# Optimization experiments

Measured on AMD Instinct MI355X. Metric: run time of the kernel, lower is better.

## Reference

```python
import jax, jax.numpy as jnp
import numpy as np

N_USERS = 100_000
N_ITEMS = 50_000
N_EDGES = 2_000_000
D = 64
ALPHA = 0.5      # tanh-blend coefficient (alpha)
NORM_2 = -1.0    # exponent on back-aggregation degree norm (args.norm_2)


def setup_inputs() -> dict:
    key = jax.random.key(0)
    k1, k2, k3, k4, k5 = jax.random.split(key, 5)
    return {
        "h_user": jax.random.normal(k1, (N_USERS, D), jnp.float32) * 0.1,
        "pretrained_feature": jax.random.normal(k2, (N_ITEMS, D), jnp.float32),
        "edge_w": jax.random.normal(k3, (N_ITEMS, 1), jnp.float32),
        "src_idx": jax.random.randint(k4, (N_EDGES,), 0, N_USERS, dtype=jnp.int32),
        "dst_idx": jax.random.randint(k5, (N_EDGES,), 0, N_ITEMS, dtype=jnp.int32),
    }


def reference(h_user, pretrained_feature, edge_w, src_idx, dst_idx):
    # HGCNLayer.forward: bidirectional copy_src+sum aggregation with degree norm,
    # tanh prompt blend and node-softmax edge weighting.
    ones = jnp.ones((N_EDGES,), h_user.dtype)

    # forward pass user -> item: rst[d] = sum_{(s,d) in E} h_user[s]
    rst = jax.ops.segment_sum(h_user[src_idx], dst_idx, num_segments=N_ITEMS)  # [N_ITEMS, D]
    deg_dst = jnp.clip(jax.ops.segment_sum(ones, dst_idx, num_segments=N_ITEMS), 1.0)

    # alpha * tanh prompt blend
    rst = rst + ALPHA * jnp.tanh(pretrained_feature)
    # edge-prompt softmax scaling (softmax over nodes; see notes)
    rst = jax.nn.softmax(edge_w, axis=0) * rst
    # in-degree^-1 normalization
    rst = rst / deg_dst[:, None]

    # backward pass item -> user: bsrc[s] = sum_{(s,d) in E} rst[d]
    bsrc = jax.ops.segment_sum(rst[dst_idx], src_idx, num_segments=N_USERS)  # [N_USERS, D]
    deg_src = jnp.clip(jax.ops.segment_sum(ones, src_idx, num_segments=N_USERS), 1.0)
    bsrc = bsrc * jnp.power(deg_src, NORM_2)[:, None]
    return bsrc
```

## Files before the change

### kernel.cpp

```cpp
#include <hip/hip_runtime.h>
#include <hip/hip_bf16.h>
#include <math.h>

#define N_USERS 100000
#define N_ITEMS 50000
#define N_EDGES 2000000
#define D 64

#define FB_BINS 98
#define BB_BINS 196
#define NBINS   (FB_BINS + BB_BINS)
#define CHUNK   4096
#define NCHUNK  ((N_EDGES + CHUNK - 1) / CHUNK)
#define FOFF_F_N (FB_BINS * 1024 + 1)
#define FOFF_B_N (BB_BINS * 512 + 1)
#define TOTSLOT  (2 * N_EDGES)
#define FWD_WGS (N_ITEMS / 16)
#define BWD_WGS ((N_USERS + 15) / 16)
#define SHARD_SPLIT 50000

__device__ __forceinline__ float blo(unsigned u) {
    union { unsigned i; float f; } c; c.i = u << 16; return c.f;
}
__device__ __forceinline__ float bhi(unsigned u) {
    union { unsigned i; float f; } c; c.i = u & 0xFFFF0000u; return c.f;
}
__device__ __forceinline__ unsigned bpack(float x, float y) {
    __hip_bfloat16 a = __float2bfloat16(x), b = __float2bfloat16(y);
    unsigned short ua = *reinterpret_cast<unsigned short*>(&a);
    unsigned short ub = *reinterpret_cast<unsigned short*>(&b);
    return (unsigned)ua | ((unsigned)ub << 16);
}

__device__ __forceinline__ void gather_run(
    const unsigned* __restrict__ tbl, const unsigned* __restrict__ stage2,
    int a, int b, int q, int half, float& ax, float& ay) {
    int k = a;
    for (; k + 16 <= b; k += 16) {
        int s0 = (int)__builtin_nontemporal_load(&stage2[k + half]);
        int s1 = (int)__builtin_nontemporal_load(&stage2[k + 2 + half]);
        int s2 = (int)__builtin_nontemporal_load(&stage2[k + 4 + half]);
        int s3 = (int)__builtin_nontemporal_load(&stage2[k + 6 + half]);
        int s4 = (int)__builtin_nontemporal_load(&stage2[k + 8 + half]);
        int s5 = (int)__builtin_nontemporal_load(&stage2[k + 10 + half]);
        int s6 = (int)__builtin_nontemporal_load(&stage2[k + 12 + half]);
        int s7 = (int)__builtin_nontemporal_load(&stage2[k + 14 + half]);
        unsigned u0 = tbl[(s0 << 5) + q];
        unsigned u1 = tbl[(s1 << 5) + q];
        unsigned u2 = tbl[(s2 << 5) + q];
        unsigned u3 = tbl[(s3 << 5) + q];
        unsigned u4 = tbl[(s4 << 5) + q];
        unsigned u5 = tbl[(s5 << 5) + q];
        unsigned u6 = tbl[(s6 << 5) + q];
        unsigned u7 = tbl[(s7 << 5) + q];
        ax += ((blo(u0) + blo(u1)) + (blo(u2) + blo(u3)))
            + ((blo(u4) + blo(u5)) + (blo(u6) + blo(u7)));
        ay += ((bhi(u0) + bhi(u1)) + (bhi(u2) + bhi(u3)))
            + ((bhi(u4) + bhi(u5)) + (bhi(u6) + bhi(u7)));
    }
    if (k + 8 <= b) {
        int s0 = (int)__builtin_nontemporal_load(&stage2[k + half]);
        int s1 = (int)__builtin_nontemporal_load(&stage2[k + 2 + half]);
        int s2 = (int)__builtin_nontemporal_load(&stage2[k + 4 + half]);
        int s3 = (int)__builtin_nontemporal_load(&stage2[k + 6 + half]);
        unsigned u0 = tbl[(s0 << 5) + q];
        unsigned u1 = tbl[(s1 << 5) + q];
        unsigned u2 = tbl[(s2 << 5) + q];
        unsigned u3 = tbl[(s3 << 5) + q];
        ax += (blo(u0) + blo(u1)) + (blo(u2) + blo(u3));
        ay += (bhi(u0) + bhi(u1)) + (bhi(u2) + bhi(u3));
        k += 8;
    }
    for (; k + 2 <= b; k += 2) {
        unsigned u = tbl[((int)__builtin_nontemporal_load(&stage2[k + half]) << 5) + q];
        ax += blo(u); ay += bhi(u);
    }
    if (k < b && half == 0) {
        unsigned u = tbl[((int)__builtin_nontemporal_load(&stage2[k]) << 5) + q];
        ax += blo(u); ay += bhi(u);
    }
}

__global__ __launch_bounds__(256) void prep_kernel(
    const float2* __restrict__ hin, unsigned* __restrict__ hu16,
    const int* __restrict__ src, const int* __restrict__ dst,
    int* __restrict__ gh) {
    __shared__ int h[NBINS];
    for (int i = threadIdx.x; i < NBINS; i += 256) h[i] = 0;
    __syncthreads();
    int stride = gridDim.x * blockDim.x;
    int t0 = blockIdx.x * blockDim.x + threadIdx.x;
    for (int i = t0; i < N_USERS * 32; i += stride) {
        float2 v = hin[i];
        hu16[i] = bpack(v.x, v.y);
    }
    for (int e = t0; e < N_EDGES; e += stride) {
        atomicAdd(&h[dst[e] >> 9], 1);
        atomicAdd(&h[FB_BINS + (src[e] >> 9)], 1);
    }
    __syncthreads();
    for (int i = threadIdx.x; i < NBINS; i += 256) {
        int v = h[i];
        if (v) atomicAdd(&gh[i], v);
    }
}

__global__ void scan_soft_kernel(const int* __restrict__ in, int* __restrict__ out,
                                 int* __restrict__ cur,
                                 const float* __restrict__ w, float* __restrict__ stats) {
    __shared__ float redf[16];
    __shared__ int wsum[16];
    int tid = threadIdx.x, lane = tid & 63, wid = tid >> 6;

    if (blockIdx.x == 0) {
        int idx0 = tid * 4;
        int v[4]; int tot = 0;
#pragma unroll
        for (int e = 0; e < 4; e++) {
            int i = idx0 + e;
            v[e] = (i < NBINS) ? in[i] : 0;
            tot += v[e];
        }
        int incl = tot;
#pragma unroll
        for (int off = 1; off < 64; off <<= 1) {
            int t = __shfl_up(incl, off);
            if (lane >= off) incl += t;
        }
        if (lane == 63) wsum[wid] = incl;
        __syncthreads();
        if (wid == 0 && lane < 16) {
            int t = wsum[lane];
            int sc = t;
#pragma unroll
            for (int off = 1; off < 16; off <<= 1) {
                int u = __shfl_up(sc, off);
                if (lane >= off) sc += u;
            }
            wsum[lane] = sc - t;
        }
        __syncthreads();
        int excl = wsum[wid] + incl - tot;
#pragma unroll
        for (int e = 0; e < 4; e++) {
            int i = idx0 + e;
            if (i < NBINS) { out[i] = excl; cur[i] = excl; }
            if (i == NBINS) out[i] = excl;
            excl += v[e];
        }
        return;
    }

    float m = -INFINITY;
    for (int i = tid; i < N_ITEMS; i += 1024) m = fmaxf(m, w[i]);
#pragma unroll
    for (int off = 32; off; off >>= 1) m = fmaxf(m, __shfl_xor(m, off));
    if (lane == 0) redf[wid] = m;
    __syncthreads();
    if (tid == 0) {
        float t = redf[0];
        for (int k = 1; k < 16; k++) t = fmaxf(t, redf[k]);
        redf[0] = t;
    }
    __syncthreads();
    m = redf[0];
    __syncthreads();

    float s = 0.f;
    for (int i = tid; i < N_ITEMS; i += 1024) s += expf(w[i] - m);
#pragma unroll
    for (int off = 32; off; off >>= 1) s += __shfl_xor(s, off);
    if (lane == 0) redf[wid] = s;
    __syncthreads();
    if (tid == 0) {
        float t = 0.f;
        for (int k = 0; k < 16; k++) t += redf[k];
        stats[0] = m;
        stats[1] = t;
    }
}

__global__ __launch_bounds__(256) void binfill_kernel(
    const int* __restrict__ src, const int* __restrict__ dst,
    int* __restrict__ gcur, unsigned* __restrict__ stage) {
    __shared__ int cnt[NBINS];
    __shared__ int gbase[NBINS];
    __shared__ int lcur[NBINS];
    int c = blockIdx.x;
    int base = c * CHUNK;
    int nEdge = N_EDGES - base; if (nEdge > CHUNK) nEdge = CHUNK;

    for (int t = threadIdx.x; t < NBINS; t += 256) { cnt[t] = 0; lcur[t] = 0; }
    __syncthreads();

    int es[16], ed[16];
#pragma unroll
    for (int j = 0; j < 16; j++) {
        int k = j * 256 + threadIdx.x;
        if (k < nEdge) {
            es[j] = src[base + k];
            ed[j] = dst[base + k];
            atomicAdd(&cnt[ed[j] >> 9], 1);
            atomicAdd(&cnt[FB_BINS + (es[j] >> 9)], 1);
        } else {
            es[j] = -1;
        }
    }
    __syncthreads();
    for (int t = threadIdx.x; t < NBINS; t += 256) {
        int cv = cnt[t];
        gbase[t] = cv ? atomicAdd(&gcur[t], cv) : 0;
    }
    __syncthreads();
#pragma unroll
    for (int j = 0; j < 16; j++) {
        if (es[j] >= 0) {
            int s = es[j], d = ed[j];
            int bf = d >> 9;
            int p = atomicAdd(&lcur[bf], 1);
            stage[gbase[bf] + p] = (unsigned)s | ((unsigned)(d & 511) << 17);
            int bb = FB_BINS + (s >> 9);
            int q = atomicAdd(&lcur[bb], 1);
            stage[gbase[bb] + q] = (unsigned)d | ((unsigned)(s & 511) << 16);
        }
    }
}

__global__ __launch_bounds__(512) void redist3_kernel(
    const unsigned* __restrict__ stage, const int* __restrict__ binoff,
    unsigned* __restrict__ stage2, int* __restrict__ foff_f, int* __restrict__ foff_b) {
    __shared__ int cnt[1024];
    __shared__ int wsum[8];
    int wg = blockIdx.x, t = threadIdx.x, lane = t & 63, wv = t >> 6;

    if (wg < FB_BINS) {
        int B = wg;
        int beg = binoff[B], end = binoff[B + 1];
        cnt[t] = 0; cnt[t + 512] = 0;
        __syncthreads();
        for (int k = beg + t; k < end; k += 512) {
            unsigned e = stage[k];
            int key = (int)((e >> 17) & 511) << 1;
            key |= ((e & 0x1FFFFu) >= SHARD_SPLIT) ? 1 : 0;
            atomicAdd(&cnt[key], 1);
        }
        __syncthreads();
        int c0 = cnt[t << 1], c1 = cnt[(t << 1) | 1];
        int v = c0 + c1;
        int incl = v;
#pragma unroll
        for (int off = 1; off < 64; off <<= 1) {
            int u = __shfl_up(incl, off);
            if (lane >= off) incl += u;
        }
        if (lane == 63) wsum[wv] = incl;
        __syncthreads();
        if (t == 0) {
            int run = 0;
#pragma unroll
            for (int k2 = 0; k2 < 8; k2++) { int x = wsum[k2]; wsum[k2] = run; run += x; }
        }
        __syncthreads();
        int base = beg + wsum[wv] + incl - v;
        int slot = (B << 10) | (t << 1);
        foff_f[slot] = base;
        foff_f[slot | 1] = base + c0;
        cnt[t << 1] = base;
        cnt[(t << 1) | 1] = base + c0;
        if (B == FB_BINS - 1 && t == 0) foff_f[FB_BINS * 1024] = end;
        __syncthreads();
        for (int k = beg + t; k < end; k += 512) {
            unsigned e = stage[k];
            int key = (int)((e >> 17) & 511) << 1;
            key |= ((e & 0x1FFFFu) >= SHARD_SPLIT) ? 1 : 0;
            int p = atomicAdd(&cnt[key], 1);
            stage2[p] = e & 0x1FFFFu;
        }
    } else {
        for (int pass = 0; pass < 2; pass++) {
            int B = FB_BINS + ((wg - FB_BINS) << 1) + pass;
            int beg = binoff[B], end = binoff[B + 1];
            cnt[t] = 0;
            __syncthreads();
            for (int k = beg + t; k < end; k += 512) {
                unsigned e = stage[k];
                atomicAdd(&cnt[(e >> 16) & 511], 1);
            }
            __syncthreads();
            int v = cnt[t];
            int incl = v;
#pragma unroll
            for (int off = 1; off < 64; off <<= 1) {
                int u = __shfl_up(incl, off);
                if (lane >= off) incl += u;
            }
            if (lane == 63) wsum[wv] = incl;
            __syncthreads();
            if (t == 0) {
                int run = 0;
#pragma unroll
                for (int k2 = 0; k2 < 8; k2++) { int x = wsum[k2]; wsum[k2] = run; run += x; }
            }
            __syncthreads();
            int base = beg + wsum[wv] + incl - v;
            foff_b[((B - FB_BINS) << 9) | t] = base;
            cnt[t] = base;
            if (B == NBINS - 1 && t == 0) foff_b[BB_BINS * 512] = end;
            __syncthreads();
            for (int k = beg + t; k < end; k += 512) {
                unsigned e = stage[k];
                int p = atomicAdd(&cnt[(e >> 16) & 511], 1);
                stage2[p] = e & 0xFFFFu;
            }
            __syncthreads();
        }
    }
}

__global__ __launch_bounds__(256) void fwd_s0_kernel(
    const unsigned* __restrict__ hu16, const unsigned* __restrict__ stage2,
    const int* __restrict__ foff_f, float* __restrict__ pacc) {
    int tid = threadIdx.x, lane = tid & 63, wv = tid >> 6;
    int q = lane & 31, half = lane >> 5;
    int i0 = blockIdx.x * 16;

    for (int il = wv; il < 16; il += 4) {
        int i = i0 + il;
        if (i >= N_ITEMS) break;
        int a = foff_f[i << 1], b = foff_f[(i << 1) | 1];
        float ax = 0.f, ay = 0.f;
        gather_run(hu16, stage2, a, b, q, half, ax, ay);
        ax += __shfl_xor(ax, 32);
        ay += __shfl_xor(ay, 32);
        if (half == 0) {
            size_t off = ((size_t)i * 32 + q) * 2;
            __builtin_nontemporal_store(ax, &pacc[off]);
            __builtin_nontemporal_store(ay, &pacc[off + 1]);
        }
    }
}

__global__ __launch_bounds__(256) void fwd_s1_kernel(
    const unsigned* __restrict__ hu16, const float* __restrict__ pf,
    const float* __restrict__ edge_w, const unsigned* __restrict__ stage2,
    const int* __restrict__ foff_f, const float* __restrict__ stats,
    const float* __restrict__ pacc, unsigned* __restrict__ rst16) {
    int tid = threadIdx.x, lane = tid & 63, wv = tid >> 6;
    int q = lane & 31, half = lane >> 5;
    float m = stats[0], ssum = stats[1];
    const float2* PF2 = (const float2*)pf;
    int i0 = blockIdx.x * 16;

    for (int il = wv; il < 16; il += 4) {
        int i = i0 + il;
        if (i >= N_ITEMS) break;
        int a = foff_f[(i << 1) | 1], b = foff_f[(i << 1) + 2];
        int a0 = foff_f[i << 1];
        float ax = 0.f, ay = 0.f;
        gather_run(hu16, stage2, a, b, q, half, ax, ay);
        ax += __shfl_xor(ax, 32);
        ay += __shfl_xor(ay, 32);
        if (half == 0) {
            size_t off = ((size_t)i * 32 + q) * 2;
            float px = __builtin_nontemporal_load(&pacc[off]);
            float py = __builtin_nontemporal_load(&pacc[off + 1]);
            ax += px; ay += py;
            float deg = (float)(b - a0);
            if (deg < 1.f) deg = 1.f;
            float sc = expf(edge_w[i] - m) / (ssum * deg);
            float2 pv = PF2[(size_t)i * 32 + q];
            float vx = (ax + 0.5f * tanhf(pv.x)) * sc;
            float vy = (ay + 0.5f * tanhf(pv.y)) * sc;
            rst16[(size_t)i * 32 + q] = bpack(vx, vy);
        }
    }
}

__global__ __launch_bounds__(256) void bwd_gather_kernel(
    const unsigned* __restrict__ rst16, const unsigned* __restrict__ stage2,
    const int* __restrict__ foff_b, float* __restrict__ out) {
    int tid = threadIdx.x, lane = tid & 63, wv = tid >> 6;
    int q = lane & 31, half = lane >> 5;
    float2* OUT2 = (float2*)out;
    int u0i = blockIdx.x * 16;

    for (int il = wv; il < 16; il += 4) {
        int u = u0i + il;
        if (u >= N_USERS) break;
        int a = foff_b[u], b = foff_b[u + 1];
        float ax = 0.f, ay = 0.f;
        gather_run(rst16, stage2, a, b, q, half, ax, ay);
        ax += __shfl_xor(ax, 32);
        ay += __shfl_xor(ay, 32);
        if (half == 0) {
            float deg = (float)(b - a);
            if (deg < 1.f) deg = 1.f;
            OUT2[(size_t)u * 32 + q] = make_float2(ax / deg, ay / deg);
        }
    }
}

extern "C" void kernel_launch(void* const* d_in, const int* in_sizes, int n_in,
                              void* d_out, int out_size, void* d_ws, size_t ws_size,
                              hipStream_t stream) {
    const float* h_user = (const float*)d_in[0];
    const float* pf     = (const float*)d_in[1];
    const float* edge_w = (const float*)d_in[2];
    const int*   src    = (const int*)d_in[3];
    const int*   dst    = (const int*)d_in[4];
    float* out = (float*)d_out;

    char* p = (char*)d_ws;
    int* gh      = (int*)p;     p += sizeof(int) * NBINS;
    int* binoff  = (int*)p;     p += sizeof(int) * (NBINS + 1);
    int* gcur    = (int*)p;     p += sizeof(int) * NBINS;
    int* foff_f  = (int*)p;     p += sizeof(int) * FOFF_F_N;
    int* foff_b  = (int*)p;     p += sizeof(int) * FOFF_B_N;
    float* stats = (float*)p;   p += 4 * sizeof(float);
    unsigned* stage  = (unsigned*)p; p += sizeof(unsigned) * (size_t)TOTSLOT;
    unsigned* stage2 = (unsigned*)p; p += sizeof(unsigned) * (size_t)TOTSLOT;
    unsigned* hu16   = (unsigned*)p; p += sizeof(unsigned) * (size_t)N_USERS * 32;
    unsigned* rst16  = (unsigned*)p; p += sizeof(unsigned) * (size_t)N_ITEMS * 32;
    float* pacc      = (float*)p;    p += sizeof(float) * (size_t)N_ITEMS * 64;

    hipMemsetAsync(gh, 0, sizeof(int) * NBINS, stream);

    prep_kernel<<<1024, 256, 0, stream>>>((const float2*)h_user, hu16, src, dst, gh);
    scan_soft_kernel<<<2, 1024, 0, stream>>>(gh, binoff, gcur, edge_w, stats);
    binfill_kernel<<<NCHUNK, 256, 0, stream>>>(src, dst, gcur, stage);
    redist3_kernel<<<196, 512, 0, stream>>>(stage, binoff, stage2, foff_f, foff_b);
    fwd_s0_kernel<<<FWD_WGS, 256, 0, stream>>>(hu16, stage2, foff_f, pacc);
    fwd_s1_kernel<<<FWD_WGS, 256, 0, stream>>>(hu16, pf, edge_w, stage2, foff_f, stats, pacc, rst16);
    bwd_gather_kernel<<<BWD_WGS, 256, 0, stream>>>(rst16, stage2, foff_b, out);
}
```

Before: 346.4 us.

## Fuse preprocessing chain into one cooperative kernel and merge forward gather shards

Four preprocessing kernels (histogram/bf16 pack, scan+softmax stats, bin fill, redistribution) become a single cooperative kernel that separates its phases with grid.sync, so the per-launch gaps between them go away. The forward gather no longer splits each item's edges into two source shards with a partial-accumulator buffer. It is now one gather kernel per item, which drops the pacc round trip and one launch. The trade-offs are grid-wide barriers, a fixed 512-block grid that loops over chunks, and the loss of the shard split that may have aided cache locality on the h_user table.

```diff
diff --git a/kernel.cpp b/kernel.cpp
--- a/kernel.cpp
+++ b/kernel.cpp
@@ -1,6 +1,9 @@
 #include <hip/hip_runtime.h>
+#include <hip/hip_cooperative_groups.h>
 #include <hip/hip_bf16.h>
 #include <math.h>
+
+namespace cg = cooperative_groups;
 
 #define N_USERS 100000
 #define N_ITEMS 50000
@@ -12,12 +15,13 @@
 #define NBINS   (FB_BINS + BB_BINS)
 #define CHUNK   4096
 #define NCHUNK  ((N_EDGES + CHUNK - 1) / CHUNK)
-#define FOFF_F_N (FB_BINS * 1024 + 1)
+#define FOFF_F_N (FB_BINS * 512 + 1)
 #define FOFF_B_N (BB_BINS * 512 + 1)
 #define TOTSLOT  (2 * N_EDGES)
+#define CHAIN_WGS 512
+#define CHAIN_THR 512
 #define FWD_WGS (N_ITEMS / 16)
 #define BWD_WGS ((N_USERS + 15) / 16)
-#define SHARD_SPLIT 50000
 
 __device__ __forceinline__ float blo(unsigned u) {
     union { unsigned i; float f; } c; c.i = u << 16; return c.f;
@@ -81,235 +85,203 @@
     }
 }
 
-__global__ __launch_bounds__(256) void prep_kernel(
+__global__ __launch_bounds__(CHAIN_THR, 4) void chain_kernel(
     const float2* __restrict__ hin, unsigned* __restrict__ hu16,
     const int* __restrict__ src, const int* __restrict__ dst,
-    int* __restrict__ gh) {
-    __shared__ int h[NBINS];
-    for (int i = threadIdx.x; i < NBINS; i += 256) h[i] = 0;
+    int* __restrict__ gh, int* __restrict__ binoff, int* __restrict__ gcur,
+    const float* __restrict__ w, float* __restrict__ stats,
+    unsigned* __restrict__ stage, unsigned* __restrict__ stage2,
+    int* __restrict__ foff_f, int* __restrict__ foff_b) {
+    cg::grid_group grid = cg::this_grid();
+    __shared__ int shA[1024];
+    __shared__ int shW[8];
+    __shared__ float shF[8];
+    int tid = threadIdx.x, lane = tid & 63, wv = tid >> 6;
+    int bx = blockIdx.x;
+    int gs = gridDim.x * CHAIN_THR;
+    int g0 = bx * CHAIN_THR + tid;
+
+    for (int i = tid; i < NBINS; i += CHAIN_THR) shA[i] = 0;
     __syncthreads();
-    int stride = gridDim.x * blockDim.x;
-    int t0 = blockIdx.x * blockDim.x + threadIdx.x;
-    for (int i = t0; i < N_USERS * 32; i += stride) {
+    for (int i = g0; i < N_USERS * 32; i += gs) {
         float2 v = hin[i];
         hu16[i] = bpack(v.x, v.y);
     }
-    for (int e = t0; e < N_EDGES; e += stride) {
-        atomicAdd(&h[dst[e] >> 9], 1);
-        atomicAdd(&h[FB_BINS + (src[e] >> 9)], 1);
+    for (int e = g0; e < N_EDGES; e += gs) {
+        atomicAdd(&shA[dst[e] >> 9], 1);
+        atomicAdd(&shA[FB_BINS + (src[e] >> 9)], 1);
     }
     __syncthreads();
-    for (int i = threadIdx.x; i < NBINS; i += 256) {
-        int v = h[i];
+    for (int i = tid; i < NBINS; i += CHAIN_THR) {
+        int v = shA[i];
         if (v) atomicAdd(&gh[i], v);
     }
-}
-
-__global__ void scan_soft_kernel(const int* __restrict__ in, int* __restrict__ out,
-                                 int* __restrict__ cur,
-                                 const float* __restrict__ w, float* __restrict__ stats) {
-    __shared__ float redf[16];
-    __shared__ int wsum[16];
-    int tid = threadIdx.x, lane = tid & 63, wid = tid >> 6;
-
-    if (blockIdx.x == 0) {
-        int idx0 = tid * 4;
-        int v[4]; int tot = 0;
-#pragma unroll
-        for (int e = 0; e < 4; e++) {
-            int i = idx0 + e;
-            v[e] = (i < NBINS) ? in[i] : 0;
-            tot += v[e];
-        }
-        int incl = tot;
+    grid.sync();
+
+    if (bx == 0) {
+        int v = (tid < NBINS) ? gh[tid] : 0;
+        int incl = v;
 #pragma unroll
         for (int off = 1; off < 64; off <<= 1) {
             int t = __shfl_up(incl, off);
             if (lane >= off) incl += t;
         }
-        if (lane == 63) wsum[wid] = incl;
-        __syncthreads();
-        if (wid == 0 && lane < 16) {
-            int t = wsum[lane];
+        if (lane == 63) shW[wv] = incl;
+        __syncthreads();
+        if (wv == 0 && lane < 8) {
+            int t = shW[lane];
             int sc = t;
 #pragma unroll
-            for (int off = 1; off < 16; off <<= 1) {
+            for (int off = 1; off < 8; off <<= 1) {
                 int u = __shfl_up(sc, off);
                 if (lane >= off) sc += u;
             }
-            wsum[lane] = sc - t;
-        }
-        __syncthreads();
-        int excl = wsum[wid] + incl - tot;
-#pragma unroll
-        for (int e = 0; e < 4; e++) {
-            int i = idx0 + e;
-            if (i < NBINS) { out[i] = excl; cur[i] = excl; }
-            if (i == NBINS) out[i] = excl;
-            excl += v[e];
-        }
-        return;
-    }
-
-    float m = -INFINITY;
-    for (int i = tid; i < N_ITEMS; i += 1024) m = fmaxf(m, w[i]);
-#pragma unroll
-    for (int off = 32; off; off >>= 1) m = fmaxf(m, __shfl_xor(m, off));
-    if (lane == 0) redf[wid] = m;
-    __syncthreads();
-    if (tid == 0) {
-        float t = redf[0];
-        for (int k = 1; k < 16; k++) t = fmaxf(t, redf[k]);
-        redf[0] = t;
-    }
-    __syncthreads();
-    m = redf[0];
-    __syncthreads();
-
-    float s = 0.f;
-    for (int i = tid; i < N_ITEMS; i += 1024) s += expf(w[i] - m);
-#pragma unroll
-    for (int off = 32; off; off >>= 1) s += __shfl_xor(s, off);
-    if (lane == 0) redf[wid] = s;
-    __syncthreads();
-    if (tid == 0) {
-        float t = 0.f;
-        for (int k = 0; k < 16; k++) t += redf[k];
-        stats[0] = m;
-        stats[1] = t;
-    }
-}
-
-__global__ __launch_bounds__(256) void binfill_kernel(
-    const int* __restrict__ src, const int* __restrict__ dst,
-    int* __restrict__ gcur, unsigned* __restrict__ stage) {
-    __shared__ int cnt[NBINS];
-    __shared__ int gbase[NBINS];
-    __shared__ int lcur[NBINS];
-    int c = blockIdx.x;
-    int base = c * CHUNK;
-    int nEdge = N_EDGES - base; if (nEdge > CHUNK) nEdge = CHUNK;
-
-    for (int t = threadIdx.x; t < NBINS; t += 256) { cnt[t] = 0; lcur[t] = 0; }
-    __syncthreads();
-
-    int es[16], ed[16];
-#pragma unroll
-    for (int j = 0; j < 16; j++) {
-        int k = j * 256 + threadIdx.x;
-        if (k < nEdge) {
-            es[j] = src[base + k];
-            ed[j] = dst[base + k];
-            atomicAdd(&cnt[ed[j] >> 9], 1);
-            atomicAdd(&cnt[FB_BINS + (es[j] >> 9)], 1);
-        } else {
-            es[j] = -1;
-        }
-    }
-    __syncthreads();
-    for (int t = threadIdx.x; t < NBINS; t += 256) {
-        int cv = cnt[t];
-        gbase[t] = cv ? atomicAdd(&gcur[t], cv) : 0;
-    }
-    __syncthreads();
-#pragma unroll
-    for (int j = 0; j < 16; j++) {
-        if (es[j] >= 0) {
-            int s = es[j], d = ed[j];
-            int bf = d >> 9;
-            int p = atomicAdd(&lcur[bf], 1);
-            stage[gbase[bf] + p] = (unsigned)s | ((unsigned)(d & 511) << 17);
-            int bb = FB_BINS + (s >> 9);
-            int q = atomicAdd(&lcur[bb], 1);
-            stage[gbase[bb] + q] = (unsigned)d | ((unsigned)(s & 511) << 16);
-        }
-    }
-}
-
-__global__ __launch_bounds__(512) void redist3_kernel(
-    const unsigned* __restrict__ stage, const int* __restrict__ binoff,
-    unsigned* __restrict__ stage2, int* __restrict__ foff_f, int* __restrict__ foff_b) {
-    __shared__ int cnt[1024];
-    __shared__ int wsum[8];
-    int wg = blockIdx.x, t = threadIdx.x, lane = t & 63, wv = t >> 6;
-
-    if (wg < FB_BINS) {
-        int B = wg;
+            shW[lane] = sc - t;
+        }
+        __syncthreads();
+        int excl = shW[wv] + incl - v;
+        if (tid < NBINS) { binoff[tid] = excl; gcur[tid] = excl; }
+        if (tid == NBINS - 1) binoff[NBINS] = excl + v;
+    } else if (bx == 1) {
+        float m = -INFINITY;
+        for (int i = tid; i < N_ITEMS; i += CHAIN_THR) m = fmaxf(m, w[i]);
+#pragma unroll
+        for (int off = 32; off; off >>= 1) m = fmaxf(m, __shfl_xor(m, off));
+        if (lane == 0) shF[wv] = m;
+        __syncthreads();
+        if (tid == 0) {
+            float t = shF[0];
+            for (int k = 1; k < 8; k++) t = fmaxf(t, shF[k]);
+            shF[0] = t;
+        }
+        __syncthreads();
+        m = shF[0];
+        __syncthreads();
+        float s = 0.f;
+        for (int i = tid; i < N_ITEMS; i += CHAIN_THR) s += expf(w[i] - m);
+#pragma unroll
+        for (int off = 32; off; off >>= 1) s += __shfl_xor(s, off);
+        if (lane == 0) shF[wv] = s;
+        __syncthreads();
+        if (tid == 0) {
+            float t = 0.f;
+            for (int k = 0; k < 8; k++) t += shF[k];
+            stats[0] = m;
+            stats[1] = t;
+        }
+    }
+    grid.sync();
+
+    {
+        int* cnt   = shA;
+        int* gbase = shA + 294;
+        int* lcur  = shA + 588;
+        for (int c = bx; c < NCHUNK; c += gridDim.x) {
+            int base = c * CHUNK;
+            int nEdge = N_EDGES - base; if (nEdge > CHUNK) nEdge = CHUNK;
+            for (int t = tid; t < NBINS; t += CHAIN_THR) { cnt[t] = 0; lcur[t] = 0; }
+            __syncthreads();
+            int es[8], ed[8];
+#pragma unroll
+            for (int j = 0; j < 8; j++) {
+                int k = j * CHAIN_THR + tid;
+                if (k < nEdge) {
+                    es[j] = src[base + k];
+                    ed[j] = dst[base + k];
+                    atomicAdd(&cnt[ed[j] >> 9], 1);
+                    atomicAdd(&cnt[FB_BINS + (es[j] >> 9)], 1);
+                } else {
+                    es[j] = -1;
+                }
+            }
+            __syncthreads();
+            for (int t = tid; t < NBINS; t += CHAIN_THR) {
+                int cv = cnt[t];
+                gbase[t] = cv ? atomicAdd(&gcur[t], cv) : 0;
+            }
+            __syncthreads();
+#pragma unroll
+            for (int j = 0; j < 8; j++) {
+                if (es[j] >= 0) {
+                    int s = es[j], d = ed[j];
+                    int bf = d >> 9;
+                    int p = atomicAdd(&lcur[bf], 1);
+                    stage[gbase[bf] + p] = (unsigned)s | ((unsigned)(d & 511) << 17);
+                    int bb = FB_BINS + (s >> 9);
+                    int qq = atomicAdd(&lcur[bb], 1);
+                    stage[gbase[bb] + qq] = (unsigned)d | ((unsigned)(s & 511) << 16);
+                }
+            }
+            __syncthreads();
+        }
+    }
+    grid.sync();
+
+    if (bx < FB_BINS) {
+        int B = bx;
         int beg = binoff[B], end = binoff[B + 1];
-        cnt[t] = 0; cnt[t + 512] = 0;
-        __syncthreads();
-        for (int k = beg + t; k < end; k += 512) {
-            unsigned e = stage[k];
-            int key = (int)((e >> 17) & 511) << 1;
-            key |= ((e & 0x1FFFFu) >= SHARD_SPLIT) ? 1 : 0;
-            atomicAdd(&cnt[key], 1);
-        }
-        __syncthreads();
-        int c0 = cnt[t << 1], c1 = cnt[(t << 1) | 1];
-        int v = c0 + c1;
+        shA[tid] = 0;
+        __syncthreads();
+        for (int k = beg + tid; k < end; k += CHAIN_THR)
+            atomicAdd(&shA[(stage[k] >> 17) & 511], 1);
+        __syncthreads();
+        int v = shA[tid];
         int incl = v;
 #pragma unroll
         for (int off = 1; off < 64; off <<= 1) {
             int u = __shfl_up(incl, off);
             if (lane >= off) incl += u;
         }
-        if (lane == 63) wsum[wv] = incl;
-        __syncthreads();
-        if (t == 0) {
+        if (lane == 63) shW[wv] = incl;
+        __syncthreads();
+        if (tid == 0) {
             int run = 0;
 #pragma unroll
-            for (int k2 = 0; k2 < 8; k2++) { int x = wsum[k2]; wsum[k2] = run; run += x; }
-        }
-        __syncthreads();
-        int base = beg + wsum[wv] + incl - v;
-        int slot = (B << 10) | (t << 1);
-        foff_f[slot] = base;
-        foff_f[slot | 1] = base + c0;
-        cnt[t << 1] = base;
-        cnt[(t << 1) | 1] = base + c0;
-        if (B == FB_BINS - 1 && t == 0) foff_f[FB_BINS * 1024] = end;
-        __syncthreads();
-        for (int k = beg + t; k < end; k += 512) {
+            for (int k2 = 0; k2 < 8; k2++) { int x = shW[k2]; shW[k2] = run; run += x; }
+        }
+        __syncthreads();
+        int base = beg + shW[wv] + incl - v;
+        foff_f[(B << 9) | tid] = base;
+        shA[tid] = base;
+        if (B == FB_BINS - 1 && tid == 0) foff_f[FB_BINS * 512] = end;
+        __syncthreads();
+        for (int k = beg + tid; k < end; k += CHAIN_THR) {
             unsigned e = stage[k];
-            int key = (int)((e >> 17) & 511) << 1;
-            key |= ((e & 0x1FFFFu) >= SHARD_SPLIT) ? 1 : 0;
-            int p = atomicAdd(&cnt[key], 1);
+            int p = atomicAdd(&shA[(e >> 17) & 511], 1);
             stage2[p] = e & 0x1FFFFu;
         }
-    } else {
+    } else if (bx < 196) {
         for (int pass = 0; pass < 2; pass++) {
-            int B = FB_BINS + ((wg - FB_BINS) << 1) + pass;
+            int B = FB_BINS + ((bx - FB_BINS) << 1) + pass;
             int beg = binoff[B], end = binoff[B + 1];
-            cnt[t] = 0;
-            __syncthreads();
-            for (int k = beg + t; k < end; k += 512) {
-                unsigned e = stage[k];
-                atomicAdd(&cnt[(e >> 16) & 511], 1);
-            }
-            __syncthreads();
-            int v = cnt[t];
+            shA[tid] = 0;
+            __syncthreads();
+            for (int k = beg + tid; k < end; k += CHAIN_THR)
+                atomicAdd(&shA[(stage[k] >> 16) & 511], 1);
+            __syncthreads();
+            int v = shA[tid];
             int incl = v;
 #pragma unroll
             for (int off = 1; off < 64; off <<= 1) {
                 int u = __shfl_up(incl, off);
                 if (lane >= off) incl += u;
             }
-            if (lane == 63) wsum[wv] = incl;
-            __syncthreads();
-            if (t == 0) {
+            if (lane == 63) shW[wv] = incl;
+            __syncthreads();
+            if (tid == 0) {
                 int run = 0;
 #pragma unroll
-                for (int k2 = 0; k2 < 8; k2++) { int x = wsum[k2]; wsum[k2] = run; run += x; }
-            }
-            __syncthreads();
-            int base = beg + wsum[wv] + incl - v;
-            foff_b[((B - FB_BINS) << 9) | t] = base;
-            cnt[t] = base;
-            if (B == NBINS - 1 && t == 0) foff_b[BB_BINS * 512] = end;
-            __syncthreads();
-            for (int k = beg + t; k < end; k += 512) {
+                for (int k2 = 0; k2 < 8; k2++) { int x = shW[k2]; shW[k2] = run; run += x; }
+            }
+            __syncthreads();
+            int base = beg + shW[wv] + incl - v;
+            foff_b[((B - FB_BINS) << 9) | tid] = base;
+            shA[tid] = base;
+            if (B == NBINS - 1 && tid == 0) foff_b[BB_BINS * 512] = end;
+            __syncthreads();
+            for (int k = beg + tid; k < end; k += CHAIN_THR) {
                 unsigned e = stage[k];
-                int p = atomicAdd(&cnt[(e >> 16) & 511], 1);
+                int p = atomicAdd(&shA[(e >> 16) & 511], 1);
                 stage2[p] = e & 0xFFFFu;
             }
             __syncthreads();
@@ -317,55 +289,27 @@
     }
 }
 
-__global__ __launch_bounds__(256) void fwd_s0_kernel(
-    const unsigned* __restrict__ hu16, const unsigned* __restrict__ stage2,
-    const int* __restrict__ foff_f, float* __restrict__ pacc) {
+__global__ __launch_bounds__(256) void fwd_gather_kernel(
+    const unsigned* __restrict__ hu16, const float* __restrict__ pf,
+    const float* __restrict__ edge_w, const unsigned* __restrict__ stage2,
+    const int* __restrict__ foff_f, const float* __restrict__ stats,
+    unsigned* __restrict__ rst16) {
     int tid = threadIdx.x, lane = tid & 63, wv = tid >> 6;
     int q = lane & 31, half = lane >> 5;
+    float m = stats[0], ssum = stats[1];
+    const float2* PF2 = (const float2*)pf;
     int i0 = blockIdx.x * 16;
 
     for (int il = wv; il < 16; il += 4) {
         int i = i0 + il;
         if (i >= N_ITEMS) break;
-        int a = foff_f[i << 1], b = foff_f[(i << 1) | 1];
+        int a = foff_f[i], b = foff_f[i + 1];
         float ax = 0.f, ay = 0.f;
         gather_run(hu16, stage2, a, b, q, half, ax, ay);
         ax += __shfl_xor(ax, 32);
         ay += __shfl_xor(ay, 32);
         if (half == 0) {
-            size_t off = ((size_t)i * 32 + q) * 2;
-            __builtin_nontemporal_store(ax, &pacc[off]);
-            __builtin_nontemporal_store(ay, &pacc[off + 1]);
-        }
-    }
-}
-
-__global__ __launch_bounds__(256) void fwd_s1_kernel(
-    const unsigned* __restrict__ hu16, const float* __restrict__ pf,
-    const float* __restrict__ edge_w, const unsigned* __restrict__ stage2,
-    const int* __restrict__ foff_f, const float* __restrict__ stats,
-    const float* __restrict__ pacc, unsigned* __restrict__ rst16) {
-    int tid = threadIdx.x, lane = tid & 63, wv = tid >> 6;
-    int q = lane & 31, half = lane >> 5;
-    float m = stats[0], ssum = stats[1];
-    const float2* PF2 = (const float2*)pf;
-    int i0 = blockIdx.x * 16;
-
-    for (int il = wv; il < 16; il += 4) {
-        int i = i0 + il;
-        if (i >= N_ITEMS) break;
-        int a = foff_f[(i << 1) | 1], b = foff_f[(i << 1) + 2];
-        int a0 = foff_f[i << 1];
-        float ax = 0.f, ay = 0.f;
-        gather_run(hu16, stage2, a, b, q, half, ax, ay);
-        ax += __shfl_xor(ax, 32);
-        ay += __shfl_xor(ay, 32);
-        if (half == 0) {
-            size_t off = ((size_t)i * 32 + q) * 2;
-            float px = __builtin_nontemporal_load(&pacc[off]);
-            float py = __builtin_nontemporal_load(&pacc[off + 1]);
-            ax += px; ay += py;
-            float deg = (float)(b - a0);
+            float deg = (float)(b - a);
             if (deg < 1.f) deg = 1.f;
             float sc = expf(edge_w[i] - m) / (ssum * deg);
             float2 pv = PF2[(size_t)i * 32 + q];
@@ -421,15 +365,19 @@
     unsigned* stage2 = (unsigned*)p; p += sizeof(unsigned) * (size_t)TOTSLOT;
     unsigned* hu16   = (unsigned*)p; p += sizeof(unsigned) * (size_t)N_USERS * 32;
     unsigned* rst16  = (unsigned*)p; p += sizeof(unsigned) * (size_t)N_ITEMS * 32;
-    float* pacc      = (float*)p;    p += sizeof(float) * (size_t)N_ITEMS * 64;
 
     hipMemsetAsync(gh, 0, sizeof(int) * NBINS, stream);
 
-    prep_kernel<<<1024, 256, 0, stream>>>((const float2*)h_user, hu16, src, dst, gh);
-    scan_soft_kernel<<<2, 1024, 0, stream>>>(gh, binoff, gcur, edge_w, stats);
-    binfill_kernel<<<NCHUNK, 256, 0, stream>>>(src, dst, gcur, stage);
-    redist3_kernel<<<196, 512, 0, stream>>>(stage, binoff, stage2, foff_f, foff_b);
-    fwd_s0_kernel<<<FWD_WGS, 256, 0, stream>>>(hu16, stage2, foff_f, pacc);
-    fwd_s1_kernel<<<FWD_WGS, 256, 0, stream>>>(hu16, pf, edge_w, stage2, foff_f, stats, pacc, rst16);
+    const float2* hin = (const float2*)h_user;
+    void* cargs[] = {
+        (void*)&hin, (void*)&hu16, (void*)&src, (void*)&dst,
+        (void*)&gh, (void*)&binoff, (void*)&gcur,
+        (void*)&edge_w, (void*)&stats,
+        (void*)&stage, (void*)&stage2, (void*)&foff_f, (void*)&foff_b
+    };
+    hipLaunchCooperativeKernel((void*)chain_kernel, dim3(CHAIN_WGS), dim3(CHAIN_THR),
+                               cargs, 0, stream);
+
+    fwd_gather_kernel<<<FWD_WGS, 256, 0, stream>>>(hu16, pf, edge_w, stage2, foff_f, stats, rst16);
     bwd_gather_kernel<<<BWD_WGS, 256, 0, stream>>>(rst16, stage2, foff_b, out);
 }
```

Measured after the change: 519.2 us. 1.5x slower.
